# Kernel optimization log

Measured on AMD Instinct MI355X. Metric: run time of the kernel, lower is better.

Reference implementation:

```python
import jax, jax.numpy as jnp
import numpy as np

N, H, D, HDIM, HID = 768, 4, 3, 64, 64


def setup_inputs() -> dict:
    key = jax.random.key(0)
    ks = jax.random.split(key, 12)

    def w(k, shape, scale=None):
        s = (1.0 / np.sqrt(shape[0])) if scale is None else scale
        return (jax.random.normal(k, shape, jnp.float32) * s).astype(jnp.float32)

    d_in_e = H + 2 * (HDIM + H * H)  # 4 + 2*(64+16) = 164
    return {
        "x": jax.random.normal(ks[0], (N, H, D), jnp.float32),
        "h": jax.random.normal(ks[1], (N, HDIM), jnp.float32),
        "phi_e_w0": w(ks[2], (d_in_e, HID)), "phi_e_b0": jnp.zeros((HID,), jnp.float32),
        "phi_e_w1": w(ks[3], (HID, HID)), "phi_e_b1": jnp.zeros((HID,), jnp.float32),
        "phi_inf_w": w(ks[4], (HID, 1)), "phi_inf_b": jnp.zeros((1,), jnp.float32),
        "phi_x_w0": w(ks[5], (HID, HID)), "phi_x_b0": jnp.zeros((HID,), jnp.float32),
        "phi_x_w1": w(ks[6], (HID, HID)), "phi_x_b1": jnp.zeros((HID,), jnp.float32),
        "phi_x_w2": w(ks[7], (HID, H), scale=0.001), "phi_x_b2": jnp.zeros((H,), jnp.float32),
        "phi_h_w0": w(ks[8], (HID + HDIM, HID)), "phi_h_b0": jnp.zeros((HID,), jnp.float32),
        "phi_h_w1": w(ks[9], (HID, HID)), "phi_h_b1": jnp.zeros((HID,), jnp.float32),
        "phi_h_w2": w(ks[10], (HID, HDIM)), "phi_h_b2": jnp.zeros((HDIM,), jnp.float32),
    }


def _mlp2(z, w0, b0, w1, b1):
    # hk.nets.MLP([HID, HID], activation=silu, activate_final=True)
    return jax.nn.silu(jax.nn.silu(z @ w0 + b0) @ w1 + b1)


def reference(x, h,
              phi_e_w0, phi_e_b0, phi_e_w1, phi_e_b1,
              phi_inf_w, phi_inf_b,
              phi_x_w0, phi_x_b0, phi_x_w1, phi_x_b1, phi_x_w2, phi_x_b2,
              phi_h_w0, phi_h_b0, phi_h_w1, phi_h_b1, phi_h_w2, phi_h_b2):
    n, n_heads = x.shape[0], x.shape[1]
    avg_num_neighbours = n - 1
    off_n = 1.0 - jnp.eye(n, dtype=x.dtype)          # zero node-diagonal mask

    # per-node head-pair differences: [n, H, H, 3], entry [m,i,j] = x[m,j]-x[m,i]
    diff_heads = x[:, None, :, :] - x[:, :, None, :]
    sq_norms_heads = jnp.sum(diff_heads ** 2, axis=-1)            # [n, H, H]
    h_concat = jnp.concatenate([h, sq_norms_heads.reshape(n, n_heads * n_heads)], axis=-1)

    # all-pairs node features: [n, n, 2*(HDIM+H^2)], entry [i,j] = [h_concat[j], h_concat[i]]
    hc_dim = h_concat.shape[-1]
    h_combos = jnp.concatenate([
        jnp.broadcast_to(h_concat[None, :, :], (n, n, hc_dim)),
        jnp.broadcast_to(h_concat[:, None, :], (n, n, hc_dim)),
    ], axis=-1)

    # all-pairs node differences per head: [n, n, H, 3], entry [i,j] = x[j]-x[i]
    diff_nodes = x[None, :, :, :] - x[:, None, :, :]
    sq_norms_nodes = jnp.sum(diff_nodes ** 2, axis=-1)            # [n, n, H]

    e_in = jnp.concatenate([sq_norms_nodes, h_combos], axis=-1)   # [n, n, 164]
    m_ij = _mlp2(e_in, phi_e_w0, phi_e_b0, phi_e_w1, phi_e_b1)    # [n, n, HID]
    m_ij = m_ij * off_n[:, :, None]

    e = jax.nn.sigmoid(m_ij @ phi_inf_w + phi_inf_b)[..., 0] * off_n  # [n, n]
    m_i = jnp.einsum('ijd,ij->id', m_ij, e) / jnp.sqrt(jnp.asarray(avg_num_neighbours, x.dtype))

    # phi_x: MLP(silu, activate_final) -> Linear(H) (tanh=False)
    phi_x_out = (_mlp2(m_ij, phi_x_w0, phi_x_b0, phi_x_w1, phi_x_b1) @ phi_x_w2 + phi_x_b2)
    phi_x_out = phi_x_out * off_n[:, :, None]                     # [n, n, H]

    # normalize_by_x_norm=True, normalization_constant=1.0
    norm = jnp.sqrt(jnp.where(sq_norms_nodes == 0.0, 1.0, sq_norms_nodes)) + 1.0
    norm_diff = (diff_nodes / norm[..., None]) * off_n[:, :, None, None]
    equivariant_shift = jnp.einsum('ijhd,ijh->ihd', norm_diff, phi_x_out)
    equivariant_shift = equivariant_shift / avg_num_neighbours    # agg='mean'

    x_new = x + equivariant_shift

    phi_h_in = jnp.concatenate([m_i, h], axis=-1)
    h_new = _mlp2(phi_h_in, phi_h_w0, phi_h_b0, phi_h_w1, phi_h_b1) @ phi_h_w2 + phi_h_b2
    h_new = h + h_new                                             # residual_h=True
    return (x_new, h_new)
```

## Files before the change

### kernel.cpp

```cpp
#include <hip/hip_runtime.h>
#include <hip/hip_bf16.h>
#include <math.h>

#define WS_BJ    0
#define WS_BI    49152
#define WS_W0AT  98304
#define WS_BIAS  98560
#define WS_INFW  98784
#define WS_WG    98848
#define WS_PM    106016
#define WS_PS    253472

typedef unsigned short ushort_t;
typedef __attribute__((ext_vector_type(8))) __bf16 bf16x8;
typedef __attribute__((ext_vector_type(4))) float f32x4;

__device__ __forceinline__ float silu_f(float v) {
    return v * __builtin_amdgcn_rcpf(1.0f + __expf(-v));
}
__device__ __forceinline__ float sigm_f(float v) {
    return __builtin_amdgcn_rcpf(1.0f + __expf(-v));
}

__device__ __forceinline__ ushort_t bf16r(float f) {
    unsigned u = __float_as_uint(f);
    u += 0x7FFFu + ((u >> 16) & 1u);
    return (ushort_t)(u >> 16);
}
__device__ __forceinline__ float bf2f(ushort_t s) { return __uint_as_float(((unsigned)s) << 16); }

__device__ __forceinline__ unsigned pk2(float a, float b) {
    __hip_bfloat162 t = __float22bfloat162_rn(make_float2(a, b));
    return *reinterpret_cast<unsigned*>(&t);
}

__global__ __launch_bounds__(256) void prep_kernel(
    const float* __restrict__ x, const float* __restrict__ h,
    const float* __restrict__ ew0, const float* __restrict__ eb0,
    const float* __restrict__ ew1, const float* __restrict__ eb1,
    const float* __restrict__ infw, const float* __restrict__ infb,
    const float* __restrict__ xw0, const float* __restrict__ xb0,
    const float* __restrict__ xw1, const float* __restrict__ xb1,
    const float* __restrict__ xw2, const float* __restrict__ xb2,
    float* __restrict__ ws)
{
    const int blk = blockIdx.x, tid = threadIdx.x;
    const int wv = tid >> 6, t = tid & 63;
    if (blk < 192) {
        __shared__ float hcs[4][80];
        const int m = blk * 4 + wv;
        hcs[wv][t] = h[m * 64 + t];
        if (t < 16) {
            int i2 = t >> 2, j2 = t & 3;
            float d0 = x[m*12 + j2*3 + 0] - x[m*12 + i2*3 + 0];
            float d1 = x[m*12 + j2*3 + 1] - x[m*12 + i2*3 + 1];
            float d2 = x[m*12 + j2*3 + 2] - x[m*12 + i2*3 + 2];
            hcs[wv][64 + t] = d0*d0 + d1*d1 + d2*d2;
        }
        float bj = 0.0f, bi = eb0[t];
        #pragma unroll 4
        for (int k = 0; k < 80; ++k) {
            float hv = hcs[wv][k];
            bj += hv * ew0[(4 + k) * 64 + t];
            bi += hv * ew0[(84 + k) * 64 + t];
        }
        ws[WS_BJ + m * 64 + t] = bj;
        ws[WS_BI + m * 64 + t] = bi;
    } else if (blk == 192) {
        if (wv == 0) {
            #pragma unroll
            for (int hh = 0; hh < 4; ++hh) ws[WS_W0AT + t * 4 + hh] = ew0[hh * 64 + t];
            ws[WS_INFW + t] = infw[t];
            #pragma unroll
            for (int u = 0; u < 4; ++u) {
                int idx = u * 64 + t;
                if (idx < 224) {
                    float v;
                    if (idx < 64)        v = eb1[idx];
                    else if (idx < 128)  v = xb0[idx - 64];
                    else if (idx == 128) v = infb[0];
                    else if (idx < 144)  v = 0.0f;
                    else if (idx < 208)  v = xb1[idx - 144];
                    else if (idx < 212)  v = xb2[idx - 208];
                    else                 v = 0.0f;
                    ws[WS_BIAS + idx] = v;
                }
            }
        }
    } else {
        ushort_t* wg = (ushort_t*)(ws + WS_WG);
        #pragma unroll 1
        for (int u = 0; u < 8; ++u) {
            int e = (blk - 193) * 2048 + tid * 8 + u;
            int r = e >> 6, k = e & 63;
            float v;
            if (r < 64)        v = ew1[k * 64 + r];
            else if (r < 128)  v = xw0[k * 64 + (r - 64)];
            else if (r == 128) v = infw[k];
            else if (r < 144)  v = 0.0f;
            else if (r < 208)  v = xw1[k * 64 + (r - 144)];
            else if (r < 212)  v = xw2[k * 4 + (r - 208)];
            else               v = 0.0f;
            wg[e] = bf16r(v);
        }
    }
}

__device__ __forceinline__ void load_bfrags(const ushort_t* yb, int ml, int q, bf16x8 B[4][2]) {
    #pragma unroll
    for (int pt = 0; pt < 4; ++pt)
        #pragma unroll
        for (int kt = 0; kt < 2; ++kt)
            B[pt][kt] = *(const bf16x8*)(yb + (pt*16 + ml) * 72 + kt*32 + q*8);
}

template<int NMT>
__device__ __forceinline__ void gemmG(const ushort_t* __restrict__ wg, int ml, int q,
                                      const bf16x8 B[4][2], f32x4* acc) {
    #pragma unroll
    for (int mt = 0; mt < NMT; ++mt) {
        #pragma unroll
        for (int kt = 0; kt < 2; ++kt) {
            bf16x8 af = *(const bf16x8*)(wg + (mt*16 + ml) * 64 + kt*32 + q*8);
            #pragma unroll
            for (int pt = 0; pt < 4; ++pt)
                acc[mt*4 + pt] = __builtin_amdgcn_mfma_f32_16x16x32_bf16(af, B[pt][kt], acc[mt*4 + pt], 0, 0, 0);
        }
    }
}

__device__ __forceinline__ void ep_silu2(ushort_t* yb, int ml, int q,
                                         const f32x4* acc, const float* __restrict__ bias,
                                         int coff) {
    #pragma unroll
    for (int mt = 0; mt < 2; ++mt) {
        float4 bv = *(const float4*)(bias + coff + mt*16 + q*4);
        #pragma unroll
        for (int pt = 0; pt < 4; ++pt) {
            f32x4 a = acc[mt*4 + pt];
            uint2 w = make_uint2(pk2(silu_f(a[0] + bv.x), silu_f(a[1] + bv.y)),
                                 pk2(silu_f(a[2] + bv.z), silu_f(a[3] + bv.w)));
            *(uint2*)(yb + (pt*16 + ml) * 72 + coff + mt*16 + q*4) = w;
        }
    }
}

__device__ __forceinline__ void layer64(ushort_t* yb, const ushort_t* __restrict__ wg,
                                        const float* __restrict__ bias, int ml, int q) {
    bf16x8 B[4][2];
    load_bfrags(yb, ml, q, B);
    f32x4 acc[8];
    #pragma unroll
    for (int t = 0; t < 8; ++t) acc[t] = f32x4{0.f, 0.f, 0.f, 0.f};
    gemmG<2>(wg, ml, q, B, acc);
    ep_silu2(yb, ml, q, acc, bias, 0);
    #pragma unroll
    for (int t = 0; t < 8; ++t) acc[t] = f32x4{0.f, 0.f, 0.f, 0.f};
    gemmG<2>(wg + 32*64, ml, q, B, acc);
    ep_silu2(yb, ml, q, acc, bias, 32);
}

__global__ __launch_bounds__(256, 2) void egcl_chunk(
    const float* __restrict__ x, float* __restrict__ ws)
{
    __shared__ ushort_t ybuf[4][4608];
    __shared__ float sbuf[4][64];
    __shared__ float redm[4][64];
    __shared__ float reds[4][12];

    const int it = blockIdx.x, i = blockIdx.y, tid = threadIdx.x;
    const int wv = tid >> 6, lane = tid & 63;
    const int ml = lane & 15, q = lane >> 4;
    const int jg = it * 256 + wv * 64 + lane;

    const ushort_t* wg = (const ushort_t*)(ws + WS_WG);
    const float* bias  = ws + WS_BIAS;
    const float* infwf = ws + WS_INFW;
    const float* Bi    = ws + WS_BI + i * 64;
    const float* w0at  = ws + WS_W0AT;
    ushort_t* yb = ybuf[wv];

    float xi[12];
    #pragma unroll
    for (int t = 0; t < 12; ++t) xi[t] = x[i * 12 + t];

    float sqn[4];
    {
        const float4* xp = (const float4*)(x + jg * 12);
        float4 a = xp[0], b = xp[1], c = xp[2];
        float d0, d1, d2;
        d0=a.x-xi[0]; d1=a.y-xi[1]; d2=a.z-xi[2];   sqn[0]=d0*d0+d1*d1+d2*d2;
        d0=a.w-xi[3]; d1=b.x-xi[4]; d2=b.y-xi[5];   sqn[1]=d0*d0+d1*d1+d2*d2;
        d0=b.z-xi[6]; d1=b.w-xi[7]; d2=c.x-xi[8];   sqn[2]=d0*d0+d1*d1+d2*d2;
        d0=c.y-xi[9]; d1=c.z-xi[10];d2=c.w-xi[11];  sqn[3]=d0*d0+d1*d1+d2*d2;
    }

    {
        const float* Bj = ws + WS_BJ + jg * 64;
        #pragma unroll
        for (int b = 0; b < 8; ++b) {
            float4 A = *(const float4*)(Bj + b*8);
            float4 Bv = *(const float4*)(Bj + b*8 + 4);
            float z[8] = {A.x, A.y, A.z, A.w, Bv.x, Bv.y, Bv.z, Bv.w};
            #pragma unroll
            for (int u = 0; u < 8; ++u) {
                int l = b*8 + u;
                float v = Bi[l] + z[u]
                        + sqn[0]*w0at[l*4+0] + sqn[1]*w0at[l*4+1]
                        + sqn[2]*w0at[l*4+2] + sqn[3]*w0at[l*4+3];
                z[u] = silu_f(v);
            }
            uint4 pkv = make_uint4(pk2(z[0],z[1]), pk2(z[2],z[3]),
                                   pk2(z[4],z[5]), pk2(z[6],z[7]));
            *(uint4*)(yb + lane * 72 + b*8) = pkv;
        }
    }

    layer64(yb, wg + 0, bias + 0, ml, q);

    {
        float sv = bias[128];
        #pragma unroll
        for (int c = 0; c < 8; ++c) {
            uint2 w0 = *(const uint2*)(yb + lane * 72 + c*8);
            uint2 w1 = *(const uint2*)(yb + lane * 72 + c*8 + 4);
            sv += __uint_as_float(w0.x << 16)          * infwf[c*8 + 0];
            sv += __uint_as_float(w0.x & 0xFFFF0000u)  * infwf[c*8 + 1];
            sv += __uint_as_float(w0.y << 16)          * infwf[c*8 + 2];
            sv += __uint_as_float(w0.y & 0xFFFF0000u)  * infwf[c*8 + 3];
            sv += __uint_as_float(w1.x << 16)          * infwf[c*8 + 4];
            sv += __uint_as_float(w1.x & 0xFFFF0000u)  * infwf[c*8 + 5];
            sv += __uint_as_float(w1.y << 16)          * infwf[c*8 + 6];
            sv += __uint_as_float(w1.y & 0xFFFF0000u)  * infwf[c*8 + 7];
        }
        sbuf[wv][lane] = (jg == i) ? 0.0f : sigm_f(sv);
    }

    float macc = 0.0f;
    #pragma unroll 8
    for (int j2 = 0; j2 < 64; ++j2) {
        float ev = sbuf[wv][j2];
        macc += ev * bf2f(yb[j2 * 72 + lane]);
    }

    layer64(yb, wg + 64*64, bias + 64, ml, q);
    layer64(yb, wg + 144*64, bias + 144, ml, q);

    float* yf = (float*)yb;
    {
        bf16x8 B[4][2];
        load_bfrags(yb, ml, q, B);
        f32x4 acc2[4];
        #pragma unroll
        for (int t = 0; t < 4; ++t) acc2[t] = f32x4{0.f, 0.f, 0.f, 0.f};
        gemmG<1>(wg + 208*64, ml, q, B, acc2);
        if (q == 0) {
            float4 bx2 = *(const float4*)(bias + 208);
            #pragma unroll
            for (int pt = 0; pt < 4; ++pt) {
                float4 pv = make_float4(acc2[pt][0] + bx2.x, acc2[pt][1] + bx2.y,
                                        acc2[pt][2] + bx2.z, acc2[pt][3] + bx2.w);
                *(float4*)(yf + (pt*16 + ml) * 4) = pv;
            }
        }
    }

    {
        float4 pv = *(const float4*)(yf + lane * 4);
        float pvh[4] = {pv.x, pv.y, pv.z, pv.w};
        float mask = (jg == i) ? 0.0f : 1.0f;
        const float4* xp = (const float4*)(x + jg * 12);
        float4 a = xp[0], b = xp[1], c = xp[2];
        float dxs[12];
        dxs[0]=a.x-xi[0]; dxs[1]=a.y-xi[1]; dxs[2]=a.z-xi[2];  dxs[3]=a.w-xi[3];
        dxs[4]=b.x-xi[4]; dxs[5]=b.y-xi[5]; dxs[6]=b.z-xi[6];  dxs[7]=b.w-xi[7];
        dxs[8]=c.x-xi[8]; dxs[9]=c.y-xi[9]; dxs[10]=c.z-xi[10];dxs[11]=c.w-xi[11];
        float s12[12];
        #pragma unroll
        for (int hh = 0; hh < 4; ++hh) {
            float nsq = (sqn[hh] == 0.0f) ? 1.0f : sqn[hh];
            float inv = mask * pvh[hh] * __builtin_amdgcn_rcpf(sqrtf(nsq) + 1.0f);
            #pragma unroll
            for (int d = 0; d < 3; ++d)
                s12[hh*3 + d] = dxs[hh*3 + d] * inv;
        }
        #pragma unroll
        for (int t = 0; t < 12; ++t) {
            float v = s12[t];
            v += __shfl_xor(v, 1, 64);
            v += __shfl_xor(v, 2, 64);
            v += __shfl_xor(v, 4, 64);
            v += __shfl_xor(v, 8, 64);
            v += __shfl_xor(v, 16, 64);
            v += __shfl_xor(v, 32, 64);
            if (lane == 0) reds[wv][t] = v;
        }
    }

    redm[wv][lane] = macc;
    __syncthreads();

    if (wv == 0) {
        ws[WS_PM + (i*3 + it)*64 + lane] =
            redm[0][lane] + redm[1][lane] + redm[2][lane] + redm[3][lane];
        if (lane < 12)
            ws[WS_PS + (i*3 + it)*12 + lane] =
                reds[0][lane] + reds[1][lane] + reds[2][lane] + reds[3][lane];
    }
}

__global__ __launch_bounds__(64) void finish_kernel(
    const float* __restrict__ x, const float* __restrict__ h,
    const float* __restrict__ hw0, const float* __restrict__ hb0,
    const float* __restrict__ hw1, const float* __restrict__ hb1,
    const float* __restrict__ hw2, const float* __restrict__ hb2,
    const float* __restrict__ ws, float* __restrict__ out)
{
    __shared__ float inbuf[128];
    __shared__ float zbuf[64];
    const int i = blockIdx.x, lane = threadIdx.x;

    const float* pm = ws + WS_PM + i*3*64;
    float mi = (pm[lane] + pm[64 + lane] + pm[128 + lane]) * (1.0f / sqrtf(767.0f));
    inbuf[lane] = mi;
    inbuf[64 + lane] = h[i*64 + lane];

    if (lane < 12) {
        const float* ps = ws + WS_PS + i*3*12;
        float sh = ps[lane] + ps[12 + lane] + ps[24 + lane];
        out[i*12 + lane] = x[i*12 + lane] + sh * (1.0f / 767.0f);
    }

    float a = hb0[lane];
    #pragma unroll 8
    for (int k = 0; k < 128; ++k) a += inbuf[k] * hw0[k*64 + lane];
    zbuf[lane] = silu_f(a);

    a = hb1[lane];
    #pragma unroll 8
    for (int k = 0; k < 64; ++k) a += zbuf[k] * hw1[k*64 + lane];
    zbuf[lane] = silu_f(a);

    a = hb2[lane];
    #pragma unroll 8
    for (int k = 0; k < 64; ++k) a += zbuf[k] * hw2[k*64 + lane];
    out[9216 + i*64 + lane] = h[i*64 + lane] + a;
}

extern "C" void kernel_launch(void* const* d_in, const int* in_sizes, int n_in,
                              void* d_out, int out_size, void* d_ws, size_t ws_size,
                              hipStream_t stream) {
    const float* x    = (const float*)d_in[0];
    const float* h    = (const float*)d_in[1];
    const float* ew0  = (const float*)d_in[2];
    const float* eb0  = (const float*)d_in[3];
    const float* ew1  = (const float*)d_in[4];
    const float* eb1  = (const float*)d_in[5];
    const float* infw = (const float*)d_in[6];
    const float* infb = (const float*)d_in[7];
    const float* xw0  = (const float*)d_in[8];
    const float* xb0  = (const float*)d_in[9];
    const float* xw1  = (const float*)d_in[10];
    const float* xb1  = (const float*)d_in[11];
    const float* xw2  = (const float*)d_in[12];
    const float* xb2  = (const float*)d_in[13];
    const float* hw0  = (const float*)d_in[14];
    const float* hb0  = (const float*)d_in[15];
    const float* hw1  = (const float*)d_in[16];
    const float* hb1  = (const float*)d_in[17];
    const float* hw2  = (const float*)d_in[18];
    const float* hb2  = (const float*)d_in[19];

    float* ws  = (float*)d_ws;
    float* out = (float*)d_out;

    prep_kernel<<<200, 256, 0, stream>>>(x, h, ew0, eb0, ew1, eb1, infw, infb,
                                         xw0, xb0, xw1, xb1, xw2, xb2, ws);
    egcl_chunk<<<dim3(3, 768), 256, 0, stream>>>(x, ws);
    finish_kernel<<<768, 64, 0, stream>>>(x, h, hw0, hb0, hw1, hb1, hw2, hb2, ws, out);
}
```

Measured before the change: 171.0 us.

## Compute first edge layer and attention logit with MFMA instead of scalar FMAs

```diff
diff --git a/kernel.cpp b/kernel.cpp
--- a/kernel.cpp
+++ b/kernel.cpp
@@ -2,18 +2,20 @@
 #include <hip/hip_bf16.h>
 #include <math.h>
 
-#define WS_BJ    0
-#define WS_BI    49152
-#define WS_W0AT  98304
-#define WS_BIAS  98560
-#define WS_INFW  98784
-#define WS_WG    98848
-#define WS_PM    106016
-#define WS_PS    253472
+#define WS_BI    0
+#define WS_BIAS  49152
+#define WS_INFW  49376
+#define WS_L0A   49440
+#define WS_WG    52512
+#define WS_BJB   59680
+#define WS_PM    84256
+#define WS_PS    231712
 
 typedef unsigned short ushort_t;
 typedef __attribute__((ext_vector_type(8))) __bf16 bf16x8;
 typedef __attribute__((ext_vector_type(4))) float f32x4;
+
+union B8U { uint4 u; bf16x8 v; };
 
 __device__ __forceinline__ float silu_f(float v) {
     return v * __builtin_amdgcn_rcpf(1.0f + __expf(-v));
@@ -64,12 +66,10 @@
             bj += hv * ew0[(4 + k) * 64 + t];
             bi += hv * ew0[(84 + k) * 64 + t];
         }
-        ws[WS_BJ + m * 64 + t] = bj;
         ws[WS_BI + m * 64 + t] = bi;
+        ((ushort_t*)(ws + WS_BJB))[m * 64 + t] = bf16r(bj);
     } else if (blk == 192) {
         if (wv == 0) {
-            #pragma unroll
-            for (int hh = 0; hh < 4; ++hh) ws[WS_W0AT + t * 4 + hh] = ew0[hh * 64 + t];
             ws[WS_INFW + t] = infw[t];
             #pragma unroll
             for (int u = 0; u < 4; ++u) {
@@ -87,7 +87,7 @@
                 }
             }
         }
-    } else {
+    } else if (blk < 200) {
         ushort_t* wg = (ushort_t*)(ws + WS_WG);
         #pragma unroll 1
         for (int u = 0; u < 8; ++u) {
@@ -103,6 +103,18 @@
             else               v = 0.0f;
             wg[e] = bf16r(v);
         }
+    } else {
+        ushort_t* l0a = (ushort_t*)(ws + WS_L0A);
+        #pragma unroll 1
+        for (int u = 0; u < 8; ++u) {
+            int e = (blk - 200) * 2048 + tid * 8 + u;
+            int r = e / 96, c = e - r * 96;
+            float v;
+            if (c < 4)       v = ew0[c * 64 + r];
+            else if (c < 32) v = 0.0f;
+            else             v = (c - 32 == r) ? 1.0f : 0.0f;
+            l0a[e] = bf16r(v);
+        }
     }
 }
 
@@ -173,11 +185,11 @@
     const int ml = lane & 15, q = lane >> 4;
     const int jg = it * 256 + wv * 64 + lane;
 
-    const ushort_t* wg = (const ushort_t*)(ws + WS_WG);
-    const float* bias  = ws + WS_BIAS;
-    const float* infwf = ws + WS_INFW;
-    const float* Bi    = ws + WS_BI + i * 64;
-    const float* w0at  = ws + WS_W0AT;
+    const ushort_t* wg  = (const ushort_t*)(ws + WS_WG);
+    const ushort_t* l0a = (const ushort_t*)(ws + WS_L0A);
+    const ushort_t* bjb = (const ushort_t*)(ws + WS_BJB);
+    const float* bias   = ws + WS_BIAS;
+    const float* BiB    = ws + WS_BI + i * 64;
     ushort_t* yb = ybuf[wv];
 
     float xi[12];
@@ -196,43 +208,52 @@
     }
 
     {
-        const float* Bj = ws + WS_BJ + jg * 64;
-        #pragma unroll
-        for (int b = 0; b < 8; ++b) {
-            float4 A = *(const float4*)(Bj + b*8);
-            float4 Bv = *(const float4*)(Bj + b*8 + 4);
-            float z[8] = {A.x, A.y, A.z, A.w, Bv.x, Bv.y, Bv.z, Bv.w};
-            #pragma unroll
-            for (int u = 0; u < 8; ++u) {
-                int l = b*8 + u;
-                float v = Bi[l] + z[u]
-                        + sqn[0]*w0at[l*4+0] + sqn[1]*w0at[l*4+1]
-                        + sqn[2]*w0at[l*4+2] + sqn[3]*w0at[l*4+3];
-                z[u] = silu_f(v);
+        *(uint2*)(yb + lane * 72 + 64) = make_uint2(pk2(sqn[0], sqn[1]), pk2(sqn[2], sqn[3]));
+
+        bf16x8 Bk[4][3];
+        const ushort_t* bjr = bjb + (size_t)(it * 256 + wv * 64) * 64;
+        #pragma unroll
+        for (int pt = 0; pt < 4; ++pt) {
+            uint2 s = *(const uint2*)(yb + (pt*16 + ml) * 72 + 64);
+            B8U u0;
+            u0.u = (q == 0) ? make_uint4(s.x, s.y, 0u, 0u) : make_uint4(0u, 0u, 0u, 0u);
+            Bk[pt][0] = u0.v;
+            Bk[pt][1] = *(const bf16x8*)(bjr + (pt*16 + ml) * 64 + q*8);
+            Bk[pt][2] = *(const bf16x8*)(bjr + (pt*16 + ml) * 64 + 32 + q*8);
+        }
+        f32x4 acc[8];
+        #pragma unroll
+        for (int half = 0; half < 2; ++half) {
+            #pragma unroll
+            for (int t = 0; t < 8; ++t) acc[t] = f32x4{0.f, 0.f, 0.f, 0.f};
+            #pragma unroll
+            for (int mt = 0; mt < 2; ++mt) {
+                #pragma unroll
+                for (int kt = 0; kt < 3; ++kt) {
+                    bf16x8 af = *(const bf16x8*)(l0a + ((half*2 + mt)*16 + ml) * 96 + kt*32 + q*8);
+                    #pragma unroll
+                    for (int pt = 0; pt < 4; ++pt)
+                        acc[mt*4 + pt] = __builtin_amdgcn_mfma_f32_16x16x32_bf16(af, Bk[pt][kt], acc[mt*4 + pt], 0, 0, 0);
+                }
             }
-            uint4 pkv = make_uint4(pk2(z[0],z[1]), pk2(z[2],z[3]),
-                                   pk2(z[4],z[5]), pk2(z[6],z[7]));
-            *(uint4*)(yb + lane * 72 + b*8) = pkv;
+            ep_silu2(yb, ml, q, acc, BiB, half * 32);
         }
     }
 
     layer64(yb, wg + 0, bias + 0, ml, q);
 
     {
-        float sv = bias[128];
-        #pragma unroll
-        for (int c = 0; c < 8; ++c) {
-            uint2 w0 = *(const uint2*)(yb + lane * 72 + c*8);
-            uint2 w1 = *(const uint2*)(yb + lane * 72 + c*8 + 4);
-            sv += __uint_as_float(w0.x << 16)          * infwf[c*8 + 0];
-            sv += __uint_as_float(w0.x & 0xFFFF0000u)  * infwf[c*8 + 1];
-            sv += __uint_as_float(w0.y << 16)          * infwf[c*8 + 2];
-            sv += __uint_as_float(w0.y & 0xFFFF0000u)  * infwf[c*8 + 3];
-            sv += __uint_as_float(w1.x << 16)          * infwf[c*8 + 4];
-            sv += __uint_as_float(w1.x & 0xFFFF0000u)  * infwf[c*8 + 5];
-            sv += __uint_as_float(w1.y << 16)          * infwf[c*8 + 6];
-            sv += __uint_as_float(w1.y & 0xFFFF0000u)  * infwf[c*8 + 7];
-        }
+        bf16x8 Bm[4][2];
+        load_bfrags(yb, ml, q, Bm);
+        f32x4 accI[4];
+        #pragma unroll
+        for (int t = 0; t < 4; ++t) accI[t] = f32x4{0.f, 0.f, 0.f, 0.f};
+        gemmG<1>(wg + 128*64, ml, q, Bm, accI);
+        if (q == 0) {
+            #pragma unroll
+            for (int pt = 0; pt < 4; ++pt) sbuf[wv][pt*16 + ml] = accI[pt][0] + bias[128];
+        }
+        float sv = sbuf[wv][lane];
         sbuf[wv][lane] = (jg == i) ? 0.0f : sigm_f(sv);
     }
 
@@ -374,7 +395,7 @@
     float* ws  = (float*)d_ws;
     float* out = (float*)d_out;
 
-    prep_kernel<<<200, 256, 0, stream>>>(x, h, ew0, eb0, ew1, eb1, infw, infb,
+    prep_kernel<<<203, 256, 0, stream>>>(x, h, ew0, eb0, ew1, eb1, infw, infb,
                                          xw0, xb0, xw1, xb1, xw2, xb2, ws);
     egcl_chunk<<<dim3(3, 768), 256, 0, stream>>>(x, ws);
     finish_kernel<<<768, 64, 0, stream>>>(x, h, hw0, hb0, hw1, hb1, hw2, hb2, ws, out);
```

Result: slower. 176.6 us (+3.3%).

## Halve rows per wave, double grid, and reduce partials with atomics

Applied to the files above, without the earlier changes.

```diff
diff --git a/kernel.cpp b/kernel.cpp
--- a/kernel.cpp
+++ b/kernel.cpp
@@ -9,7 +9,7 @@
 #define WS_INFW  98784
 #define WS_WG    98848
 #define WS_PM    106016
-#define WS_PS    253472
+#define WS_PS    155168
 
 typedef unsigned short ushort_t;
 typedef __attribute__((ext_vector_type(8))) __bf16 bf16x8;
@@ -87,7 +87,7 @@
                 }
             }
         }
-    } else {
+    } else if (blk < 200) {
         ushort_t* wg = (ushort_t*)(ws + WS_WG);
         #pragma unroll 1
         for (int u = 0; u < 8; ++u) {
@@ -103,81 +103,74 @@
             else               v = 0.0f;
             wg[e] = bf16r(v);
         }
-    }
-}
-
-__device__ __forceinline__ void load_bfrags(const ushort_t* yb, int ml, int q, bf16x8 B[4][2]) {
-    #pragma unroll
-    for (int pt = 0; pt < 4; ++pt)
+    } else {
+        int e = (blk - 200) * 256 + tid;
+        if (e < 58368) ws[WS_PM + e] = 0.0f;
+    }
+}
+
+__device__ __forceinline__ void load_bfrags2(const ushort_t* yb, int ml, int q, bf16x8 B[2][2]) {
+    #pragma unroll
+    for (int pt = 0; pt < 2; ++pt)
         #pragma unroll
         for (int kt = 0; kt < 2; ++kt)
             B[pt][kt] = *(const bf16x8*)(yb + (pt*16 + ml) * 72 + kt*32 + q*8);
 }
 
 template<int NMT>
-__device__ __forceinline__ void gemmG(const ushort_t* __restrict__ wg, int ml, int q,
-                                      const bf16x8 B[4][2], f32x4* acc) {
+__device__ __forceinline__ void gemm2(const ushort_t* __restrict__ wg, int ml, int q,
+                                      const bf16x8 B[2][2], f32x4* acc) {
     #pragma unroll
     for (int mt = 0; mt < NMT; ++mt) {
         #pragma unroll
         for (int kt = 0; kt < 2; ++kt) {
             bf16x8 af = *(const bf16x8*)(wg + (mt*16 + ml) * 64 + kt*32 + q*8);
             #pragma unroll
-            for (int pt = 0; pt < 4; ++pt)
-                acc[mt*4 + pt] = __builtin_amdgcn_mfma_f32_16x16x32_bf16(af, B[pt][kt], acc[mt*4 + pt], 0, 0, 0);
-        }
-    }
-}
-
-__device__ __forceinline__ void ep_silu2(ushort_t* yb, int ml, int q,
-                                         const f32x4* acc, const float* __restrict__ bias,
-                                         int coff) {
-    #pragma unroll
-    for (int mt = 0; mt < 2; ++mt) {
-        float4 bv = *(const float4*)(bias + coff + mt*16 + q*4);
-        #pragma unroll
-        for (int pt = 0; pt < 4; ++pt) {
-            f32x4 a = acc[mt*4 + pt];
+            for (int pt = 0; pt < 2; ++pt)
+                acc[mt*2 + pt] = __builtin_amdgcn_mfma_f32_16x16x32_bf16(af, B[pt][kt], acc[mt*2 + pt], 0, 0, 0);
+        }
+    }
+}
+
+__device__ __forceinline__ void layer32(ushort_t* yb, const ushort_t* __restrict__ wg,
+                                        const float* __restrict__ bias, int ml, int q) {
+    bf16x8 B[2][2];
+    load_bfrags2(yb, ml, q, B);
+    f32x4 acc[8];
+    #pragma unroll
+    for (int t = 0; t < 8; ++t) acc[t] = f32x4{0.f, 0.f, 0.f, 0.f};
+    gemm2<4>(wg, ml, q, B, acc);
+    #pragma unroll
+    for (int mt = 0; mt < 4; ++mt) {
+        float4 bv = *(const float4*)(bias + mt*16 + q*4);
+        #pragma unroll
+        for (int pt = 0; pt < 2; ++pt) {
+            f32x4 a = acc[mt*2 + pt];
             uint2 w = make_uint2(pk2(silu_f(a[0] + bv.x), silu_f(a[1] + bv.y)),
                                  pk2(silu_f(a[2] + bv.z), silu_f(a[3] + bv.w)));
-            *(uint2*)(yb + (pt*16 + ml) * 72 + coff + mt*16 + q*4) = w;
-        }
-    }
-}
-
-__device__ __forceinline__ void layer64(ushort_t* yb, const ushort_t* __restrict__ wg,
-                                        const float* __restrict__ bias, int ml, int q) {
-    bf16x8 B[4][2];
-    load_bfrags(yb, ml, q, B);
-    f32x4 acc[8];
-    #pragma unroll
-    for (int t = 0; t < 8; ++t) acc[t] = f32x4{0.f, 0.f, 0.f, 0.f};
-    gemmG<2>(wg, ml, q, B, acc);
-    ep_silu2(yb, ml, q, acc, bias, 0);
-    #pragma unroll
-    for (int t = 0; t < 8; ++t) acc[t] = f32x4{0.f, 0.f, 0.f, 0.f};
-    gemmG<2>(wg + 32*64, ml, q, B, acc);
-    ep_silu2(yb, ml, q, acc, bias, 32);
+            *(uint2*)(yb + (pt*16 + ml) * 72 + mt*16 + q*4) = w;
+        }
+    }
 }
 
 __global__ __launch_bounds__(256, 2) void egcl_chunk(
     const float* __restrict__ x, float* __restrict__ ws)
 {
-    __shared__ ushort_t ybuf[4][4608];
-    __shared__ float sbuf[4][64];
+    __shared__ ushort_t ybuf[4][2304];
+    __shared__ float sbuf[4][32];
+    __shared__ float pbuf[4][128];
     __shared__ float redm[4][64];
     __shared__ float reds[4][12];
 
     const int it = blockIdx.x, i = blockIdx.y, tid = threadIdx.x;
     const int wv = tid >> 6, lane = tid & 63;
     const int ml = lane & 15, q = lane >> 4;
-    const int jg = it * 256 + wv * 64 + lane;
+    const int p = lane & 31, half = lane >> 5;
+    const int jg = it * 128 + wv * 32 + p;
 
     const ushort_t* wg = (const ushort_t*)(ws + WS_WG);
     const float* bias  = ws + WS_BIAS;
     const float* infwf = ws + WS_INFW;
-    const float* Bi    = ws + WS_BI + i * 64;
-    const float* w0at  = ws + WS_W0AT;
     ushort_t* yb = ybuf[wv];
 
     float xi[12];
@@ -196,34 +189,37 @@
     }
 
     {
-        const float* Bj = ws + WS_BJ + jg * 64;
-        #pragma unroll
-        for (int b = 0; b < 8; ++b) {
-            float4 A = *(const float4*)(Bj + b*8);
-            float4 Bv = *(const float4*)(Bj + b*8 + 4);
-            float z[8] = {A.x, A.y, A.z, A.w, Bv.x, Bv.y, Bv.z, Bv.w};
+        const float* BiL = ws + WS_BI + i * 64 + half * 32;
+        const float* BjL = ws + WS_BJ + jg * 64 + half * 32;
+        const float* w0L = ws + WS_W0AT + half * 128;
+        #pragma unroll
+        for (int b = 0; b < 4; ++b) {
+            float4 bi0 = *(const float4*)(BiL + b*8);
+            float4 bi1 = *(const float4*)(BiL + b*8 + 4);
+            float4 bj0 = *(const float4*)(BjL + b*8);
+            float4 bj1 = *(const float4*)(BjL + b*8 + 4);
+            float z[8] = {bi0.x+bj0.x, bi0.y+bj0.y, bi0.z+bj0.z, bi0.w+bj0.w,
+                          bi1.x+bj1.x, bi1.y+bj1.y, bi1.z+bj1.z, bi1.w+bj1.w};
             #pragma unroll
             for (int u = 0; u < 8; ++u) {
-                int l = b*8 + u;
-                float v = Bi[l] + z[u]
-                        + sqn[0]*w0at[l*4+0] + sqn[1]*w0at[l*4+1]
-                        + sqn[2]*w0at[l*4+2] + sqn[3]*w0at[l*4+3];
+                float4 w = *(const float4*)(w0L + (b*8 + u) * 4);
+                float v = z[u] + sqn[0]*w.x + sqn[1]*w.y + sqn[2]*w.z + sqn[3]*w.w;
                 z[u] = silu_f(v);
             }
             uint4 pkv = make_uint4(pk2(z[0],z[1]), pk2(z[2],z[3]),
                                    pk2(z[4],z[5]), pk2(z[6],z[7]));
-            *(uint4*)(yb + lane * 72 + b*8) = pkv;
-        }
-    }
-
-    layer64(yb, wg + 0, bias + 0, ml, q);
+            *(uint4*)(yb + p * 72 + half * 32 + b*8) = pkv;
+        }
+    }
+
+    layer32(yb, wg + 0, bias + 0, ml, q);
 
     {
         float sv = bias[128];
         #pragma unroll
         for (int c = 0; c < 8; ++c) {
-            uint2 w0 = *(const uint2*)(yb + lane * 72 + c*8);
-            uint2 w1 = *(const uint2*)(yb + lane * 72 + c*8 + 4);
+            uint2 w0 = *(const uint2*)(yb + p * 72 + c*8);
+            uint2 w1 = *(const uint2*)(yb + p * 72 + c*8 + 4);
             sv += __uint_as_float(w0.x << 16)          * infwf[c*8 + 0];
             sv += __uint_as_float(w0.x & 0xFFFF0000u)  * infwf[c*8 + 1];
             sv += __uint_as_float(w0.y << 16)          * infwf[c*8 + 2];
@@ -233,67 +229,61 @@
             sv += __uint_as_float(w1.y << 16)          * infwf[c*8 + 6];
             sv += __uint_as_float(w1.y & 0xFFFF0000u)  * infwf[c*8 + 7];
         }
-        sbuf[wv][lane] = (jg == i) ? 0.0f : sigm_f(sv);
+        if (half == 0) sbuf[wv][p] = (jg == i) ? 0.0f : sigm_f(sv);
     }
 
     float macc = 0.0f;
     #pragma unroll 8
-    for (int j2 = 0; j2 < 64; ++j2) {
+    for (int j2 = 0; j2 < 32; ++j2) {
         float ev = sbuf[wv][j2];
         macc += ev * bf2f(yb[j2 * 72 + lane]);
     }
 
-    layer64(yb, wg + 64*64, bias + 64, ml, q);
-    layer64(yb, wg + 144*64, bias + 144, ml, q);
-
-    float* yf = (float*)yb;
-    {
-        bf16x8 B[4][2];
-        load_bfrags(yb, ml, q, B);
-        f32x4 acc2[4];
-        #pragma unroll
-        for (int t = 0; t < 4; ++t) acc2[t] = f32x4{0.f, 0.f, 0.f, 0.f};
-        gemmG<1>(wg + 208*64, ml, q, B, acc2);
+    layer32(yb, wg + 64*64, bias + 64, ml, q);
+    layer32(yb, wg + 144*64, bias + 144, ml, q);
+
+    {
+        bf16x8 B[2][2];
+        load_bfrags2(yb, ml, q, B);
+        f32x4 acc2[2];
+        #pragma unroll
+        for (int t = 0; t < 2; ++t) acc2[t] = f32x4{0.f, 0.f, 0.f, 0.f};
+        gemm2<1>(wg + 208*64, ml, q, B, acc2);
         if (q == 0) {
             float4 bx2 = *(const float4*)(bias + 208);
             #pragma unroll
-            for (int pt = 0; pt < 4; ++pt) {
+            for (int pt = 0; pt < 2; ++pt) {
                 float4 pv = make_float4(acc2[pt][0] + bx2.x, acc2[pt][1] + bx2.y,
                                         acc2[pt][2] + bx2.z, acc2[pt][3] + bx2.w);
-                *(float4*)(yf + (pt*16 + ml) * 4) = pv;
+                *(float4*)(pbuf[wv] + (pt*16 + ml) * 4) = pv;
             }
         }
     }
 
     {
-        float4 pv = *(const float4*)(yf + lane * 4);
-        float pvh[4] = {pv.x, pv.y, pv.z, pv.w};
         float mask = (jg == i) ? 0.0f : 1.0f;
-        const float4* xp = (const float4*)(x + jg * 12);
-        float4 a = xp[0], b = xp[1], c = xp[2];
-        float dxs[12];
-        dxs[0]=a.x-xi[0]; dxs[1]=a.y-xi[1]; dxs[2]=a.z-xi[2];  dxs[3]=a.w-xi[3];
-        dxs[4]=b.x-xi[4]; dxs[5]=b.y-xi[5]; dxs[6]=b.z-xi[6];  dxs[7]=b.w-xi[7];
-        dxs[8]=c.x-xi[8]; dxs[9]=c.y-xi[9]; dxs[10]=c.z-xi[10];dxs[11]=c.w-xi[11];
-        float s12[12];
-        #pragma unroll
-        for (int hh = 0; hh < 4; ++hh) {
+        const float* xj = x + jg * 12 + half * 6;
+        const float* xih = xi + half * 6;
+        float s6[6];
+        #pragma unroll
+        for (int hl = 0; hl < 2; ++hl) {
+            int hh = half * 2 + hl;
+            float pv = pbuf[wv][p * 4 + hh];
             float nsq = (sqn[hh] == 0.0f) ? 1.0f : sqn[hh];
-            float inv = mask * pvh[hh] * __builtin_amdgcn_rcpf(sqrtf(nsq) + 1.0f);
+            float inv = mask * pv * __builtin_amdgcn_rcpf(sqrtf(nsq) + 1.0f);
             #pragma unroll
             for (int d = 0; d < 3; ++d)
-                s12[hh*3 + d] = dxs[hh*3 + d] * inv;
-        }
-        #pragma unroll
-        for (int t = 0; t < 12; ++t) {
-            float v = s12[t];
+                s6[hl*3 + d] = (xj[hl*3 + d] - xih[hl*3 + d]) * inv;
+        }
+        #pragma unroll
+        for (int t = 0; t < 6; ++t) {
+            float v = s6[t];
             v += __shfl_xor(v, 1, 64);
             v += __shfl_xor(v, 2, 64);
             v += __shfl_xor(v, 4, 64);
             v += __shfl_xor(v, 8, 64);
             v += __shfl_xor(v, 16, 64);
-            v += __shfl_xor(v, 32, 64);
-            if (lane == 0) reds[wv][t] = v;
+            if (p == 0) reds[wv][half*6 + t] = v;
         }
     }
 
@@ -301,11 +291,12 @@
     __syncthreads();
 
     if (wv == 0) {
-        ws[WS_PM + (i*3 + it)*64 + lane] =
-            redm[0][lane] + redm[1][lane] + redm[2][lane] + redm[3][lane];
-        if (lane < 12)
-            ws[WS_PS + (i*3 + it)*12 + lane] =
-                reds[0][lane] + reds[1][lane] + reds[2][lane] + reds[3][lane];
+        float tm = redm[0][lane] + redm[1][lane] + redm[2][lane] + redm[3][lane];
+        atomicAdd(&ws[WS_PM + i*64 + lane], tm);
+        if (lane < 12) {
+            float tsv = reds[0][lane] + reds[1][lane] + reds[2][lane] + reds[3][lane];
+            atomicAdd(&ws[WS_PS + i*12 + lane], tsv);
+        }
     }
 }
 
@@ -320,14 +311,12 @@
     __shared__ float zbuf[64];
     const int i = blockIdx.x, lane = threadIdx.x;
 
-    const float* pm = ws + WS_PM + i*3*64;
-    float mi = (pm[lane] + pm[64 + lane] + pm[128 + lane]) * (1.0f / sqrtf(767.0f));
+    float mi = ws[WS_PM + i*64 + lane] * (1.0f / sqrtf(767.0f));
     inbuf[lane] = mi;
     inbuf[64 + lane] = h[i*64 + lane];
 
     if (lane < 12) {
-        const float* ps = ws + WS_PS + i*3*12;
-        float sh = ps[lane] + ps[12 + lane] + ps[24 + lane];
+        float sh = ws[WS_PS + i*12 + lane];
         out[i*12 + lane] = x[i*12 + lane] + sh * (1.0f / 767.0f);
     }
 
@@ -374,8 +363,8 @@
     float* ws  = (float*)d_ws;
     float* out = (float*)d_out;
 
-    prep_kernel<<<200, 256, 0, stream>>>(x, h, ew0, eb0, ew1, eb1, infw, infb,
+    prep_kernel<<<428, 256, 0, stream>>>(x, h, ew0, eb0, ew1, eb1, infw, infb,
                                          xw0, xb0, xw1, xb1, xw2, xb2, ws);
-    egcl_chunk<<<dim3(3, 768), 256, 0, stream>>>(x, ws);
+    egcl_chunk<<<dim3(6, 768), 256, 0, stream>>>(x, ws);
     finish_kernel<<<768, 64, 0, stream>>>(x, h, hw0, hb0, hw1, hb1, hw2, hb2, ws, out);
 }
```

After: 211.5 us. 1.24x slower.

## Fuse attention gate into first edge layer and use atomics for node reductions

Applied to the files above, without the earlier changes.

```diff
diff --git a/kernel.cpp b/kernel.cpp
--- a/kernel.cpp
+++ b/kernel.cpp
@@ -9,7 +9,7 @@
 #define WS_INFW  98784
 #define WS_WG    98848
 #define WS_PM    106016
-#define WS_PS    253472
+#define WS_PS    155168
 
 typedef unsigned short ushort_t;
 typedef __attribute__((ext_vector_type(8))) __bf16 bf16x8;
@@ -27,7 +27,6 @@
     u += 0x7FFFu + ((u >> 16) & 1u);
     return (ushort_t)(u >> 16);
 }
-__device__ __forceinline__ float bf2f(ushort_t s) { return __uint_as_float(((unsigned)s) << 16); }
 
 __device__ __forceinline__ unsigned pk2(float a, float b) {
     __hip_bfloat162 t = __float22bfloat162_rn(make_float2(a, b));
@@ -87,7 +86,7 @@
                 }
             }
         }
-    } else {
+    } else if (blk < 200) {
         ushort_t* wg = (ushort_t*)(ws + WS_WG);
         #pragma unroll 1
         for (int u = 0; u < 8; ++u) {
@@ -103,6 +102,9 @@
             else               v = 0.0f;
             wg[e] = bf16r(v);
         }
+    } else {
+        int e = (blk - 200) * 256 + tid;
+        if (e < 58368) ws[WS_PM + e] = 0.0f;
     }
 }
 
@@ -129,44 +131,42 @@
     }
 }
 
-__device__ __forceinline__ void ep_silu2(ushort_t* yb, int ml, int q,
-                                         const f32x4* acc, const float* __restrict__ bias,
-                                         int coff) {
+__device__ __forceinline__ void acc_bias(f32x4* acc, const float* __restrict__ bias,
+                                         int coff, int q) {
     #pragma unroll
     for (int mt = 0; mt < 2; ++mt) {
         float4 bv = *(const float4*)(bias + coff + mt*16 + q*4);
         #pragma unroll
-        for (int pt = 0; pt < 4; ++pt) {
-            f32x4 a = acc[mt*4 + pt];
-            uint2 w = make_uint2(pk2(silu_f(a[0] + bv.x), silu_f(a[1] + bv.y)),
-                                 pk2(silu_f(a[2] + bv.z), silu_f(a[3] + bv.w)));
-            *(uint2*)(yb + (pt*16 + ml) * 72 + coff + mt*16 + q*4) = w;
-        }
-    }
-}
-
-__device__ __forceinline__ void layer64(ushort_t* yb, const ushort_t* __restrict__ wg,
-                                        const float* __restrict__ bias, int ml, int q) {
-    bf16x8 B[4][2];
-    load_bfrags(yb, ml, q, B);
+        for (int pt = 0; pt < 4; ++pt)
+            acc[mt*4 + pt] = f32x4{bv.x, bv.y, bv.z, bv.w};
+    }
+}
+
+__device__ __forceinline__ void layer64B(ushort_t* yb, const ushort_t* __restrict__ wg,
+                                         const float* __restrict__ bias, int ml, int q,
+                                         const bf16x8 B[4][2]) {
     f32x4 acc[8];
     #pragma unroll
-    for (int t = 0; t < 8; ++t) acc[t] = f32x4{0.f, 0.f, 0.f, 0.f};
-    gemmG<2>(wg, ml, q, B, acc);
-    ep_silu2(yb, ml, q, acc, bias, 0);
-    #pragma unroll
-    for (int t = 0; t < 8; ++t) acc[t] = f32x4{0.f, 0.f, 0.f, 0.f};
-    gemmG<2>(wg + 32*64, ml, q, B, acc);
-    ep_silu2(yb, ml, q, acc, bias, 32);
+    for (int half = 0; half < 2; ++half) {
+        acc_bias(acc, bias, half*32, q);
+        gemmG<2>(wg + half*32*64, ml, q, B, acc);
+        #pragma unroll
+        for (int mt = 0; mt < 2; ++mt) {
+            #pragma unroll
+            for (int pt = 0; pt < 4; ++pt) {
+                f32x4 a = acc[mt*4 + pt];
+                uint2 w = make_uint2(pk2(silu_f(a[0]), silu_f(a[1])),
+                                     pk2(silu_f(a[2]), silu_f(a[3])));
+                *(uint2*)(yb + (pt*16 + ml) * 72 + half*32 + mt*16 + q*4) = w;
+            }
+        }
+    }
 }
 
 __global__ __launch_bounds__(256, 2) void egcl_chunk(
     const float* __restrict__ x, float* __restrict__ ws)
 {
     __shared__ ushort_t ybuf[4][4608];
-    __shared__ float sbuf[4][64];
-    __shared__ float redm[4][64];
-    __shared__ float reds[4][12];
 
     const int it = blockIdx.x, i = blockIdx.y, tid = threadIdx.x;
     const int wv = tid >> 6, lane = tid & 63;
@@ -176,8 +176,6 @@
     const ushort_t* wg = (const ushort_t*)(ws + WS_WG);
     const float* bias  = ws + WS_BIAS;
     const float* infwf = ws + WS_INFW;
-    const float* Bi    = ws + WS_BI + i * 64;
-    const float* w0at  = ws + WS_W0AT;
     ushort_t* yb = ybuf[wv];
 
     float xi[12];
@@ -196,7 +194,9 @@
     }
 
     {
-        const float* Bj = ws + WS_BJ + jg * 64;
+        const float* Bi   = ws + WS_BI + i * 64;
+        const float* w0at = ws + WS_W0AT;
+        const float* Bj   = ws + WS_BJ + jg * 64;
         #pragma unroll
         for (int b = 0; b < 8; ++b) {
             float4 A = *(const float4*)(Bj + b*8);
@@ -216,52 +216,78 @@
         }
     }
 
-    layer64(yb, wg + 0, bias + 0, ml, q);
-
-    {
-        float sv = bias[128];
-        #pragma unroll
-        for (int c = 0; c < 8; ++c) {
-            uint2 w0 = *(const uint2*)(yb + lane * 72 + c*8);
-            uint2 w1 = *(const uint2*)(yb + lane * 72 + c*8 + 4);
-            sv += __uint_as_float(w0.x << 16)          * infwf[c*8 + 0];
-            sv += __uint_as_float(w0.x & 0xFFFF0000u)  * infwf[c*8 + 1];
-            sv += __uint_as_float(w0.y << 16)          * infwf[c*8 + 2];
-            sv += __uint_as_float(w0.y & 0xFFFF0000u)  * infwf[c*8 + 3];
-            sv += __uint_as_float(w1.x << 16)          * infwf[c*8 + 4];
-            sv += __uint_as_float(w1.x & 0xFFFF0000u)  * infwf[c*8 + 5];
-            sv += __uint_as_float(w1.y << 16)          * infwf[c*8 + 6];
-            sv += __uint_as_float(w1.y & 0xFFFF0000u)  * infwf[c*8 + 7];
-        }
-        sbuf[wv][lane] = (jg == i) ? 0.0f : sigm_f(sv);
-    }
-
-    float macc = 0.0f;
-    #pragma unroll 8
-    for (int j2 = 0; j2 < 64; ++j2) {
-        float ev = sbuf[wv][j2];
-        macc += ev * bf2f(yb[j2 * 72 + lane]);
-    }
-
-    layer64(yb, wg + 64*64, bias + 64, ml, q);
-    layer64(yb, wg + 144*64, bias + 144, ml, q);
+    bf16x8 B[4][2];
+
+    float infp[4] = {0.f, 0.f, 0.f, 0.f};
+    {
+        load_bfrags(yb, ml, q, B);
+        f32x4 acc[8];
+        #pragma unroll
+        for (int half = 0; half < 2; ++half) {
+            acc_bias(acc, bias + 0, half*32, q);
+            gemmG<2>(wg + half*32*64, ml, q, B, acc);
+            #pragma unroll
+            for (int mt = 0; mt < 2; ++mt) {
+                float4 iw = *(const float4*)(infwf + half*32 + mt*16 + q*4);
+                #pragma unroll
+                for (int pt = 0; pt < 4; ++pt) {
+                    f32x4 a = acc[mt*4 + pt];
+                    float s0 = silu_f(a[0]), s1 = silu_f(a[1]);
+                    float s2 = silu_f(a[2]), s3 = silu_f(a[3]);
+                    infp[pt] += s0*iw.x + s1*iw.y + s2*iw.z + s3*iw.w;
+                    *(uint2*)(yb + (pt*16 + ml) * 72 + half*32 + mt*16 + q*4) =
+                        make_uint2(pk2(s0, s1), pk2(s2, s3));
+                }
+            }
+        }
+    }
+
+    float e4[4];
+    {
+        float binf = bias[128];
+        #pragma unroll
+        for (int pt = 0; pt < 4; ++pt) {
+            float v = infp[pt];
+            v += __shfl_xor(v, 16, 64);
+            v += __shfl_xor(v, 32, 64);
+            int jp = it * 256 + wv * 64 + pt*16 + ml;
+            e4[pt] = (jp == i) ? 0.0f : sigm_f(v + binf);
+        }
+    }
+
+    float macc[16];
+    load_bfrags(yb, ml, q, B);
+    #pragma unroll
+    for (int kt = 0; kt < 2; ++kt) {
+        #pragma unroll
+        for (int j = 0; j < 8; ++j) {
+            float s = e4[0] * (float)B[0][kt][j];
+            s      += e4[1] * (float)B[1][kt][j];
+            s      += e4[2] * (float)B[2][kt][j];
+            s      += e4[3] * (float)B[3][kt][j];
+            macc[kt*8 + j] = s;
+        }
+    }
+    layer64B(yb, wg + 64*64, bias + 64, ml, q, B);
+
+    load_bfrags(yb, ml, q, B);
+    layer64B(yb, wg + 144*64, bias + 144, ml, q, B);
 
     float* yf = (float*)yb;
     {
-        bf16x8 B[4][2];
         load_bfrags(yb, ml, q, B);
         f32x4 acc2[4];
-        #pragma unroll
-        for (int t = 0; t < 4; ++t) acc2[t] = f32x4{0.f, 0.f, 0.f, 0.f};
+        {
+            float4 bx2 = *(const float4*)(bias + 208);
+            #pragma unroll
+            for (int pt = 0; pt < 4; ++pt) acc2[pt] = f32x4{bx2.x, bx2.y, bx2.z, bx2.w};
+        }
         gemmG<1>(wg + 208*64, ml, q, B, acc2);
         if (q == 0) {
-            float4 bx2 = *(const float4*)(bias + 208);
-            #pragma unroll
-            for (int pt = 0; pt < 4; ++pt) {
-                float4 pv = make_float4(acc2[pt][0] + bx2.x, acc2[pt][1] + bx2.y,
-                                        acc2[pt][2] + bx2.z, acc2[pt][3] + bx2.w);
-                *(float4*)(yf + (pt*16 + ml) * 4) = pv;
-            }
+            #pragma unroll
+            for (int pt = 0; pt < 4; ++pt)
+                *(float4*)(yf + (pt*16 + ml) * 4) =
+                    make_float4(acc2[pt][0], acc2[pt][1], acc2[pt][2], acc2[pt][3]);
         }
     }
 
@@ -293,19 +319,25 @@
             v += __shfl_xor(v, 8, 64);
             v += __shfl_xor(v, 16, 64);
             v += __shfl_xor(v, 32, 64);
-            if (lane == 0) reds[wv][t] = v;
-        }
-    }
-
-    redm[wv][lane] = macc;
-    __syncthreads();
-
-    if (wv == 0) {
-        ws[WS_PM + (i*3 + it)*64 + lane] =
-            redm[0][lane] + redm[1][lane] + redm[2][lane] + redm[3][lane];
-        if (lane < 12)
-            ws[WS_PS + (i*3 + it)*12 + lane] =
-                reds[0][lane] + reds[1][lane] + reds[2][lane] + reds[3][lane];
+            if (lane == 0) atomicAdd(&ws[WS_PS + i*12 + t], v);
+        }
+    }
+
+    #pragma unroll
+    for (int s = 0; s < 16; ++s) {
+        float v = macc[s];
+        v += __shfl_xor(v, 1, 64);
+        v += __shfl_xor(v, 2, 64);
+        v += __shfl_xor(v, 4, 64);
+        v += __shfl_xor(v, 8, 64);
+        macc[s] = v;
+    }
+    if (ml == 0) {
+        #pragma unroll
+        for (int kt = 0; kt < 2; ++kt)
+            #pragma unroll
+            for (int j = 0; j < 8; ++j)
+                atomicAdd(&ws[WS_PM + i*64 + kt*32 + q*8 + j], macc[kt*8 + j]);
     }
 }
 
@@ -320,14 +352,12 @@
     __shared__ float zbuf[64];
     const int i = blockIdx.x, lane = threadIdx.x;
 
-    const float* pm = ws + WS_PM + i*3*64;
-    float mi = (pm[lane] + pm[64 + lane] + pm[128 + lane]) * (1.0f / sqrtf(767.0f));
+    float mi = ws[WS_PM + i*64 + lane] * (1.0f / sqrtf(767.0f));
     inbuf[lane] = mi;
     inbuf[64 + lane] = h[i*64 + lane];
 
     if (lane < 12) {
-        const float* ps = ws + WS_PS + i*3*12;
-        float sh = ps[lane] + ps[12 + lane] + ps[24 + lane];
+        float sh = ws[WS_PS + i*12 + lane];
         out[i*12 + lane] = x[i*12 + lane] + sh * (1.0f / 767.0f);
     }
 
@@ -374,7 +404,7 @@
     float* ws  = (float*)d_ws;
     float* out = (float*)d_out;
 
-    prep_kernel<<<200, 256, 0, stream>>>(x, h, ew0, eb0, ew1, eb1, infw, infb,
+    prep_kernel<<<428, 256, 0, stream>>>(x, h, ew0, eb0, ew1, eb1, infw, infb,
                                          xw0, xb0, xw1, xb1, xw2, xb2, ws);
     egcl_chunk<<<dim3(3, 768), 256, 0, stream>>>(x, ws);
     finish_kernel<<<768, 64, 0, stream>>>(x, h, hw0, hb0, hw1, hb1, hw2, hb2, ws, out);
```

Measured after the change: 190.9 us. 11.7% more time.
